# Optimization experiments

Measured on AMD Instinct MI355X. Metric: run time of the kernel, lower is better.

Reference implementation:

```python
import jax, jax.numpy as jnp
import numpy as np
from jax import lax

D, H, DH, F, K, L, N = 512, 8, 64, 2048, 31, 512, 16
EPS = 1e-5

def layer_norm(x, g, b):
    m = x.mean(-1, keepdims=True)
    v = ((x - m) ** 2).mean(-1, keepdims=True)
    return (x - m) / jnp.sqrt(v + EPS) * g + b

def swish(x):
    return x * jax.nn.sigmoid(x)

def ffn(x, w1, b1, w2, b2):
    return swish(x @ w1.T + b1) @ w2.T + b2

def rel_shift(x):
    # x: (N,H,T,2T-1) -> (N,H,T,T); out[...,i,j] = x[...,i, T-1-i+j]
    T = x.shape[2]
    rows = jnp.arange(T)[:, None]
    cols = (T - 1) - rows + jnp.arange(T)[None, :]
    return x[:, :, rows, cols]

def rel_attn(x, pos_emb, in_w, in_b, out_w, out_b, pos_w, bu, bv):
    Lq, Nb, E = x.shape
    qkv = x @ in_w.T + in_b  # (L,N,3E)
    q, k, v = jnp.split(qkv, 3, axis=-1)
    q = q.reshape(Lq, Nb, H, DH).transpose(1, 2, 0, 3)  # (N,H,L,DH)
    k = k.reshape(Lq, Nb, H, DH).transpose(1, 2, 0, 3)
    v = v.reshape(Lq, Nb, H, DH).transpose(1, 2, 0, 3)
    p = (pos_emb[0] @ pos_w.T).reshape(-1, H, DH).transpose(1, 0, 2)  # (H,2L-1,DH)
    scaling = DH ** -0.5
    q_u = q + bu[None, :, None, :]
    q_v = q + bv[None, :, None, :]
    matrix_ac = jnp.einsum('nhld,nhsd->nhls', q_u, k)        # (N,H,L,L)
    matrix_bd = jnp.einsum('nhld,hmd->nhlm', q_v, p)         # (N,H,L,2L-1)
    matrix_bd = rel_shift(matrix_bd)                         # (N,H,L,L)
    attn = jax.nn.softmax((matrix_ac + matrix_bd) * scaling, axis=-1)
    out = jnp.einsum('nhls,nhsd->nhld', attn, v)
    out = out.transpose(2, 0, 1, 3).reshape(Lq, Nb, E)
    return out @ out_w.T + out_b

def conv_module(x, pw1_w, pw1_b, dw_w, dw_b, g, b, mean, var, pw2_w, pw2_b):
    # x: (L,N,C) -> (N,C,L)
    y = x.transpose(1, 2, 0)
    y = jnp.einsum('ncl,oc->nol', y, pw1_w) + pw1_b[None, :, None]
    a, gate = jnp.split(y, 2, axis=1)
    y = a * jax.nn.sigmoid(gate)  # GLU over channel dim
    pad = (K - 1) // 2
    y = lax.conv_general_dilated(y, dw_w[:, None, :], (1,), [(pad, pad)],
                                 feature_group_count=D,
                                 dimension_numbers=('NCH', 'OIH', 'NCH'))
    y = y + dw_b[None, :, None]
    # BatchNorm1d in eval mode with running stats
    y = (y - mean[None, :, None]) / jnp.sqrt(var[None, :, None] + EPS)
    y = y * g[None, :, None] + b[None, :, None]
    y = swish(y)
    y = jnp.einsum('ncl,oc->nol', y, pw2_w) + pw2_b[None, :, None]
    return y.transpose(2, 0, 1)  # back to (L,N,C)

def setup_inputs() -> dict:
    key = jax.random.key(0)
    ks = iter(jax.random.split(key, 64))
    def nrm(shape, s=0.02):
        return jax.random.normal(next(ks), shape, dtype=jnp.float32) * s
    return {
        'src': jax.random.normal(next(ks), (L, N, D), dtype=jnp.float32),
        'pos_emb': jax.random.normal(next(ks), (1, 2 * L - 1, D), dtype=jnp.float32),
        'ffm_w1': nrm((F, D)), 'ffm_b1': jnp.zeros((F,), jnp.float32),
        'ffm_w2': nrm((D, F)), 'ffm_b2': jnp.zeros((D,), jnp.float32),
        'ff_w1': nrm((F, D)), 'ff_b1': jnp.zeros((F,), jnp.float32),
        'ff_w2': nrm((D, F)), 'ff_b2': jnp.zeros((D,), jnp.float32),
        'in_proj_w': nrm((3 * D, D)), 'in_proj_b': jnp.zeros((3 * D,), jnp.float32),
        'out_proj_w': nrm((D, D)), 'out_proj_b': jnp.zeros((D,), jnp.float32),
        'pos_w': nrm((D, D)),
        'pos_bias_u': nrm((H, DH)), 'pos_bias_v': nrm((H, DH)),
        'conv_pw1_w': nrm((2 * D, D)), 'conv_pw1_b': jnp.zeros((2 * D,), jnp.float32),
        'conv_dw_w': nrm((D, K)), 'conv_dw_b': jnp.zeros((D,), jnp.float32),
        'bn_gamma': jnp.ones((D,), jnp.float32), 'bn_beta': jnp.zeros((D,), jnp.float32),
        'bn_mean': jnp.zeros((D,), jnp.float32), 'bn_var': jnp.ones((D,), jnp.float32),
        'conv_pw2_w': nrm((D, D)), 'conv_pw2_b': jnp.zeros((D,), jnp.float32),
        'ln_ffm_g': jnp.ones((D,), jnp.float32), 'ln_ffm_b': jnp.zeros((D,), jnp.float32),
        'ln_mha_g': jnp.ones((D,), jnp.float32), 'ln_mha_b': jnp.zeros((D,), jnp.float32),
        'ln_conv_g': jnp.ones((D,), jnp.float32), 'ln_conv_b': jnp.zeros((D,), jnp.float32),
        'ln_ff_g': jnp.ones((D,), jnp.float32), 'ln_ff_b': jnp.zeros((D,), jnp.float32),
        'ln_final_g': jnp.ones((D,), jnp.float32), 'ln_final_b': jnp.zeros((D,), jnp.float32),
    }

def reference(src, pos_emb, ffm_w1, ffm_b1, ffm_w2, ffm_b2, ff_w1, ff_b1, ff_w2, ff_b2,
              in_proj_w, in_proj_b, out_proj_w, out_proj_b, pos_w, pos_bias_u, pos_bias_v,
              conv_pw1_w, conv_pw1_b, conv_dw_w, conv_dw_b, bn_gamma, bn_beta, bn_mean, bn_var,
              conv_pw2_w, conv_pw2_b, ln_ffm_g, ln_ffm_b, ln_mha_g, ln_mha_b, ln_conv_g, ln_conv_b,
              ln_ff_g, ln_ff_b, ln_final_g, ln_final_b):
    # pre-norm conformer block, ff_scale = 0.5, dropout omitted (eval)
    x = src
    x = x + 0.5 * ffn(layer_norm(x, ln_ffm_g, ln_ffm_b), ffm_w1, ffm_b1, ffm_w2, ffm_b2)
    x = x + rel_attn(layer_norm(x, ln_mha_g, ln_mha_b), pos_emb,
                     in_proj_w, in_proj_b, out_proj_w, out_proj_b,
                     pos_w, pos_bias_u, pos_bias_v)
    x = x + conv_module(layer_norm(x, ln_conv_g, ln_conv_b),
                        conv_pw1_w, conv_pw1_b, conv_dw_w, conv_dw_b,
                        bn_gamma, bn_beta, bn_mean, bn_var, conv_pw2_w, conv_pw2_b)
    x = x + 0.5 * ffn(layer_norm(x, ln_ff_g, ln_ff_b), ff_w1, ff_b1, ff_w2, ff_b2)
    return layer_norm(x, ln_final_g, ln_final_b)
```

## Files before the change

### kernel.cpp

```cpp
#include <hip/hip_runtime.h>
#include <cstdint>
#include <cstddef>

typedef unsigned short u16;
typedef __attribute__((ext_vector_type(4))) float f32x4;
typedef __attribute__((ext_vector_type(8))) short bf16x8;
typedef __attribute__((ext_vector_type(8))) unsigned short u16x8;

__device__ __forceinline__ float sigm(float x) { return 1.f / (1.f + __expf(-x)); }
__device__ __forceinline__ float bf2f(u16 u) {
    union { unsigned int i; float f; } c; c.i = ((unsigned int)u) << 16; return c.f;
}
__device__ __forceinline__ u16 f2bf(float f) {
    union { float f; unsigned int i; } c; c.f = f;
    unsigned int x = c.i;
    x += 0x7fffu + ((x >> 16) & 1u);
    return (u16)(x >> 16);
}


__global__ void castall_k(const float* __restrict__ s0, const float* __restrict__ s1,
                          const float* __restrict__ s2, const float* __restrict__ s3,
                          const float* __restrict__ s4, const float* __restrict__ s5,
                          const float* __restrict__ s6, const float* __restrict__ s7,
                          const float* __restrict__ s8, const float* __restrict__ s9,
                          u16* __restrict__ dst) {
    int i = blockIdx.x * 256 + threadIdx.x;
    if (i >= 6815232) return;
    const float* s; int off;
    if      (i < 1048576) { s = s0; off = 0; }
    else if (i < 2097152) { s = s1; off = 1048576; }
    else if (i < 3145728) { s = s2; off = 2097152; }
    else if (i < 4194304) { s = s3; off = 3145728; }
    else if (i < 4980736) { s = s4; off = 4194304; }
    else if (i < 5242880) { s = s5; off = 4980736; }
    else if (i < 5767168) { s = s6; off = 5242880; }
    else if (i < 6029312) { s = s7; off = 5767168; }
    else if (i < 6291456) { s = s8; off = 6029312; }
    else                  { s = s9; off = 6291456; }
    dst[i] = f2bf(s[i - off]);
}

template <bool OUTBF>
__global__ __launch_bounds__(256) void ln512_k(const float* __restrict__ x,
                                               const float* __restrict__ g,
                                               const float* __restrict__ b,
                                               void* __restrict__ outv) {
    int row = blockIdx.x * 4 + (threadIdx.x >> 6);
    int lane = threadIdx.x & 63;
    const float* xr = x + (size_t)row * 512 + lane * 8;
    float4 v0 = *(const float4*)(xr);
    float4 v1 = *(const float4*)(xr + 4);
    float va[8] = {v0.x, v0.y, v0.z, v0.w, v1.x, v1.y, v1.z, v1.w};
    float s = 0.f;
#pragma unroll
    for (int t = 0; t < 8; t++) s += va[t];
#pragma unroll
    for (int o = 32; o > 0; o >>= 1) s += __shfl_xor(s, o);
    float m = s * (1.0f / 512.0f);
    float q = 0.f;
#pragma unroll
    for (int t = 0; t < 8; t++) { float d = va[t] - m; q += d * d; }
#pragma unroll
    for (int o = 32; o > 0; o >>= 1) q += __shfl_xor(q, o);
    float inv = rsqrtf(q * (1.0f / 512.0f) + 1e-5f);
    int cb = lane * 8;
    if (OUTBF) {
        u16* o = (u16*)outv + (size_t)row * 512 + cb;
#pragma unroll
        for (int t = 0; t < 8; t++)
            o[t] = f2bf((va[t] - m) * inv * g[cb + t] + b[cb + t]);
    } else {
        float* o = (float*)outv + (size_t)row * 512 + cb;
#pragma unroll
        for (int t = 0; t < 8; t++)
            o[t] = (va[t] - m) * inv * g[cb + t] + b[cb + t];
    }
}

__global__ __launch_bounds__(512) void mgemm_k(
    const u16* __restrict__ A, const u16* __restrict__ B, const float* __restrict__ bias,
    const float* __restrict__ add, void* __restrict__ Cv,
    int M, int Nn, int Kk, float coef, int act, int outbf) {
    __shared__ u16 lA[2][4096];
    __shared__ u16 lB[2][4096];
    int tid = threadIdx.x;
    int half = tid >> 8;
    int t128 = tid & 255;
    int lane = tid & 63;
    int w = (tid >> 6) & 3;
    int wm = (w >> 1) * 64, wn = (w & 1) * 64;
    int m0 = blockIdx.x << 7, n0 = blockIdx.y << 7;
    int Kh = Kk >> 1;
    int kbase = half * Kh;

    f32x4 acc[4][4];
#pragma unroll
    for (int i = 0; i < 4; i++)
#pragma unroll
        for (int j = 0; j < 4; j++) acc[i][j] = (f32x4){0.f, 0.f, 0.f, 0.f};

    int srow = t128 >> 2;
    int scol = (t128 & 3) << 3;
    const u16* gA = A + (size_t)(m0 + srow) * Kk + kbase + scol;
    const u16* gB = B + (size_t)(n0 + srow) * Kk + kbase + scol;
    int lso = t128 * 8;

    int lra = wm * 32 + (lane & 15) * 32 + (lane >> 4) * 8;
    int lrb = wn * 32 + (lane & 15) * 32 + (lane >> 4) * 8;

    for (int k0 = 0; k0 < Kh; k0 += 32) {
        __builtin_amdgcn_global_load_lds(
            (const __attribute__((address_space(1))) void*)(gA + k0),
            (__attribute__((address_space(3))) void*)(lA[half] + lso), 16, 0, 0);
        __builtin_amdgcn_global_load_lds(
            (const __attribute__((address_space(1))) void*)(gA + (size_t)64 * Kk + k0),
            (__attribute__((address_space(3))) void*)(lA[half] + 2048 + lso), 16, 0, 0);
        __builtin_amdgcn_global_load_lds(
            (const __attribute__((address_space(1))) void*)(gB + k0),
            (__attribute__((address_space(3))) void*)(lB[half] + lso), 16, 0, 0);
        __builtin_amdgcn_global_load_lds(
            (const __attribute__((address_space(1))) void*)(gB + (size_t)64 * Kk + k0),
            (__attribute__((address_space(3))) void*)(lB[half] + 2048 + lso), 16, 0, 0);
        __syncthreads();
        bf16x8 af[4], bf[4];
#pragma unroll
        for (int t = 0; t < 4; t++) {
            af[t] = *(const bf16x8*)(lA[half] + lra + t * 512);
            bf[t] = *(const bf16x8*)(lB[half] + lrb + t * 512);
        }
#pragma unroll
        for (int i = 0; i < 4; i++)
#pragma unroll
            for (int j = 0; j < 4; j++)
                acc[i][j] = __builtin_amdgcn_mfma_f32_16x16x32_bf16(af[i], bf[j], acc[i][j], 0, 0, 0);
        __syncthreads();
    }

    float* red = (float*)lA;
#pragma unroll
    for (int rr = 0; rr < 4; rr++) {
        if (half == 1) {
#pragma unroll
            for (int j = 0; j < 4; j++)
                *(f32x4*)(red + ((w * 64 + lane) * 16 + j * 4)) = acc[rr][j];
        }
        __syncthreads();
        if (half == 0) {
#pragma unroll
            for (int j = 0; j < 4; j++) {
                f32x4 o = *(const f32x4*)(red + ((w * 64 + lane) * 16 + j * 4));
                acc[rr][j] += o;
            }
        }
        __syncthreads();
    }

    if (half == 0) {
        int rbase = (lane >> 4) * 4;
        int ncol = lane & 15;
#pragma unroll
        for (int i = 0; i < 4; i++) {
#pragma unroll
            for (int j = 0; j < 4; j++) {
                int n = n0 + wn + j * 16 + ncol;
                float bv = bias ? bias[n] : 0.f;
#pragma unroll
                for (int r = 0; r < 4; r++) {
                    int m = m0 + wm + i * 16 + rbase + r;
                    float c = acc[i][j][r] + bv;
                    if (act == 1) c *= sigm(c);
                    size_t o = (size_t)m * Nn + n;
                    if (add) c = add[o] + coef * c;
                    if (outbf) ((u16*)Cv)[o] = f2bf(c);
                    else ((float*)Cv)[o] = c;
                }
            }
        }
    }
}

__global__ __launch_bounds__(256) void posb_k(const u16* __restrict__ A,
                                              const u16* __restrict__ B,
                                              u16* __restrict__ Pbf) {
    __shared__ u16 lA[4096];
    __shared__ u16 lB[4096];
    const int Kk = 512;
    int tid = threadIdx.x;
    int lane = tid & 63, w = tid >> 6;
    int wm = (w >> 1) * 64, wn = (w & 1) * 64;
    int m0 = blockIdx.x << 7, n0 = blockIdx.y << 7;

    f32x4 acc[4][4];
#pragma unroll
    for (int i = 0; i < 4; i++)
#pragma unroll
        for (int j = 0; j < 4; j++) acc[i][j] = (f32x4){0.f, 0.f, 0.f, 0.f};

    int srow = tid >> 2;
    int scol = (tid & 3) << 3;
    int ar0 = m0 + srow;       if (ar0 > 1022) ar0 = 1022;
    int ar1 = m0 + 64 + srow;  if (ar1 > 1022) ar1 = 1022;
    const u16* gA0 = A + (size_t)ar0 * Kk + scol;
    const u16* gA1 = A + (size_t)ar1 * Kk + scol;
    const u16* gB = B + (size_t)(n0 + srow) * Kk + scol;
    int lso = tid * 8;
    int lra = wm * 32 + (lane & 15) * 32 + (lane >> 4) * 8;
    int lrb = wn * 32 + (lane & 15) * 32 + (lane >> 4) * 8;

    for (int k0 = 0; k0 < Kk; k0 += 32) {
        __builtin_amdgcn_global_load_lds(
            (const __attribute__((address_space(1))) void*)(gA0 + k0),
            (__attribute__((address_space(3))) void*)(lA + lso), 16, 0, 0);
        __builtin_amdgcn_global_load_lds(
            (const __attribute__((address_space(1))) void*)(gA1 + k0),
            (__attribute__((address_space(3))) void*)(lA + 2048 + lso), 16, 0, 0);
        __builtin_amdgcn_global_load_lds(
            (const __attribute__((address_space(1))) void*)(gB + k0),
            (__attribute__((address_space(3))) void*)(lB + lso), 16, 0, 0);
        __builtin_amdgcn_global_load_lds(
            (const __attribute__((address_space(1))) void*)(gB + (size_t)64 * Kk + k0),
            (__attribute__((address_space(3))) void*)(lB + 2048 + lso), 16, 0, 0);
        __syncthreads();
        bf16x8 af[4], bf[4];
#pragma unroll
        for (int t = 0; t < 4; t++) {
            af[t] = *(const bf16x8*)(lA + lra + t * 512);
            bf[t] = *(const bf16x8*)(lB + lrb + t * 512);
        }
#pragma unroll
        for (int i = 0; i < 4; i++)
#pragma unroll
            for (int j = 0; j < 4; j++)
                acc[i][j] = __builtin_amdgcn_mfma_f32_16x16x32_bf16(af[i], bf[j], acc[i][j], 0, 0, 0);
        __syncthreads();
    }

    int rbase = (lane >> 4) * 4;
    int ncol = lane & 15;
#pragma unroll
    for (int i = 0; i < 4; i++) {
#pragma unroll
        for (int j = 0; j < 4; j++) {
            int n = n0 + wn + j * 16 + ncol;
            int h = n >> 6, d = n & 63;
#pragma unroll
            for (int r = 0; r < 4; r++) {
                int m = m0 + wm + i * 16 + rbase + r;
                u16 val = (m < 1023) ? f2bf(acc[i][j][r]) : (u16)0;
                Pbf[(((size_t)(h * 1024 + m)) << 6) + d] = val;
            }
        }
    }
}

__global__ __launch_bounds__(256) void fattn_k(
    const u16* __restrict__ QU, const u16* __restrict__ QV,
    const u16* __restrict__ Kb, const u16* __restrict__ Pbf,
    const u16* __restrict__ VT, u16* __restrict__ ctx) {
    __shared__ u16 arr[26496];
    u16* sB = arr;
    u16* sV = arr;
    u16* sRect = arr + 16896;
    u16* sP = arr + 16896;
    u16* sQ = arr + 25344;
    u16* sCtx = arr + 25344;
    float* sRed = (float*)(arr + 26368);

    int tid = threadIdx.x;
    int lane = tid & 63, w = tid >> 6;
    int quad = lane >> 4, col = lane & 15;
    int nh = blockIdx.x, h = nh & 7, nb = nh >> 3;
    int m0 = blockIdx.y << 4;
    int nlo = 496 - m0;

    if (tid < 128)
        __builtin_amdgcn_global_load_lds(
            (const __attribute__((address_space(1))) void*)(QV + (((size_t)nh * 512 + m0 + (tid >> 3)) << 6) + ((tid & 7) << 3)),
            (__attribute__((address_space(3))) void*)(sQ + tid * 8), 16, 0, 0);
    f32x4 bdacc[9];
#pragma unroll
    for (int i = 0; i < 9; i++) bdacc[i] = (f32x4){0.f, 0.f, 0.f, 0.f};
    const u16* Pb = Pbf + ((size_t)h << 16);
    for (int ks = 0; ks < 2; ks++) {
#pragma unroll
        for (int s = 0; s < 8; s++) {
            int row = (s << 6) + (tid >> 2);
            __builtin_amdgcn_global_load_lds(
                (const __attribute__((address_space(1))) void*)(Pb + (((size_t)(nlo + row)) << 6) + (ks << 5) + ((tid & 3) << 3)),
                (__attribute__((address_space(3))) void*)(sB + (s << 11) + tid * 8), 16, 0, 0);
        }
        if (tid < 64) {
            int row = 512 + (tid >> 2);
            __builtin_amdgcn_global_load_lds(
                (const __attribute__((address_space(1))) void*)(Pb + (((size_t)(nlo + row)) << 6) + (ks << 5) + ((tid & 3) << 3)),
                (__attribute__((address_space(3))) void*)(sB + (8 << 11) + tid * 8), 16, 0, 0);
        }
        __syncthreads();
        bf16x8 a = *(const bf16x8*)(sQ + col * 64 + (ks << 5) + quad * 8);
#pragma unroll
        for (int idx = 0; idx < 9; idx++) {
            int nt = w + (idx << 2);
            if (nt < 33) {
                bf16x8 b = *(const bf16x8*)(sB + ((nt * 16 + col) << 5) + quad * 8);
                bdacc[idx] = __builtin_amdgcn_mfma_f32_16x16x32_bf16(a, b, bdacc[idx], 0, 0, 0);
            }
        }
        __syncthreads();
    }
#pragma unroll
    for (int idx = 0; idx < 9; idx++) {
        int nt = w + (idx << 2);
        if (nt < 33) {
            int c = nt * 16 + col;
#pragma unroll
            for (int r = 0; r < 4; r++) {
                int ml = quad * 4 + r;
                int j = c + ml - 15;
                if (j >= 0 && j < 512)
                    sRect[ml * 524 + j] = f2bf(bdacc[idx][r]);
            }
        }
    }
    __syncthreads();

    if (tid < 128)
        __builtin_amdgcn_global_load_lds(
            (const __attribute__((address_space(1))) void*)(QU + (((size_t)nh * 512 + m0 + (tid >> 3)) << 6) + ((tid & 7) << 3)),
            (__attribute__((address_space(3))) void*)(sQ + tid * 8), 16, 0, 0);
    f32x4 ac[8];
#pragma unroll
    for (int i = 0; i < 8; i++) ac[i] = (f32x4){0.f, 0.f, 0.f, 0.f};
    const u16* Kz = Kb + ((size_t)nh << 15);
    for (int ks = 0; ks < 2; ks++) {
#pragma unroll
        for (int s = 0; s < 8; s++) {
            int row = (s << 6) + (tid >> 2);
            __builtin_amdgcn_global_load_lds(
                (const __attribute__((address_space(1))) void*)(Kz + ((size_t)row << 6) + (ks << 5) + ((tid & 3) << 3)),
                (__attribute__((address_space(3))) void*)(sB + (s << 11) + tid * 8), 16, 0, 0);
        }
        __syncthreads();
        bf16x8 a = *(const bf16x8*)(sQ + col * 64 + (ks << 5) + quad * 8);
#pragma unroll
        for (int jt = 0; jt < 8; jt++) {
            bf16x8 b = *(const bf16x8*)(sB + (((w << 7) + jt * 16 + col) << 5) + quad * 8);
            ac[jt] = __builtin_amdgcn_mfma_f32_16x16x32_bf16(a, b, ac[jt], 0, 0, 0);
        }
        __syncthreads();
    }

    float rmax[4];
#pragma unroll
    for (int r = 0; r < 4; r++) rmax[r] = -1e30f;
#pragma unroll
    for (int jt = 0; jt < 8; jt++) {
        int j = (w << 7) + jt * 16 + col;
#pragma unroll
        for (int r = 0; r < 4; r++) {
            int ml = quad * 4 + r;
            float v = (ac[jt][r] + bf2f(sRect[ml * 524 + j])) * 0.125f;
            ac[jt][r] = v;
            rmax[r] = fmaxf(rmax[r], v);
        }
    }
#pragma unroll
    for (int o = 1; o <= 8; o <<= 1)
#pragma unroll
        for (int r = 0; r < 4; r++) rmax[r] = fmaxf(rmax[r], __shfl_xor(rmax[r], o));
    if (col == 0)
#pragma unroll
        for (int r = 0; r < 4; r++) sRed[(quad * 4 + r) * 4 + w] = rmax[r];
    __syncthreads();
    float gmax[4], psum[4];
#pragma unroll
    for (int r = 0; r < 4; r++) {
        int ml = quad * 4 + r;
        gmax[r] = fmaxf(fmaxf(sRed[ml * 4 + 0], sRed[ml * 4 + 1]),
                        fmaxf(sRed[ml * 4 + 2], sRed[ml * 4 + 3]));
        psum[r] = 0.f;
    }
    __syncthreads();
#pragma unroll
    for (int jt = 0; jt < 8; jt++)
#pragma unroll
        for (int r = 0; r < 4; r++) {
            float e = __expf(ac[jt][r] - gmax[r]);
            ac[jt][r] = e;
            psum[r] += e;
        }
#pragma unroll
    for (int o = 1; o <= 8; o <<= 1)
#pragma unroll
        for (int r = 0; r < 4; r++) psum[r] += __shfl_xor(psum[r], o);
    if (col == 0)
#pragma unroll
        for (int r = 0; r < 4; r++) sRed[(quad * 4 + r) * 4 + w] = psum[r];
    __syncthreads();
    float rinv[4];
#pragma unroll
    for (int r = 0; r < 4; r++) {
        int ml = quad * 4 + r;
        rinv[r] = 1.f / (sRed[ml * 4 + 0] + sRed[ml * 4 + 1] + sRed[ml * 4 + 2] + sRed[ml * 4 + 3]);
    }

#pragma unroll
    for (int jt = 0; jt < 8; jt++) {
        int j = (w << 7) + jt * 16 + col;
#pragma unroll
        for (int r = 0; r < 4; r++)
            sP[(quad * 4 + r) * 520 + j] = f2bf(ac[jt][r] * rinv[r]);
    }

    const u16* Vz = VT + ((size_t)nh << 15);
    f32x4 cacc = (f32x4){0.f, 0.f, 0.f, 0.f};
    for (int kc = 0; kc < 2; kc++) {
#pragma unroll
        for (int s = 0; s < 8; s++) {
            int d = (s << 3) + (tid >> 5);
            int chunk = (tid & 31) ^ (d & 7);
            __builtin_amdgcn_global_load_lds(
                (const __attribute__((address_space(1))) void*)(Vz + ((size_t)d << 9) + (kc << 8) + (chunk << 3)),
                (__attribute__((address_space(3))) void*)(sV + (s << 11) + tid * 8), 16, 0, 0);
        }
        __syncthreads();
#pragma unroll
        for (int s2 = 0; s2 < 8; s2++) {
            bf16x8 a = *(const bf16x8*)(sP + col * 520 + (kc << 8) + (s2 << 5) + quad * 8);
            int row = (w << 4) + col;
            int ch = ((s2 << 2) + quad) ^ (col & 7);
            bf16x8 b = *(const bf16x8*)(sV + (row << 8) + (ch << 3));
            cacc = __builtin_amdgcn_mfma_f32_16x16x32_bf16(a, b, cacc, 0, 0, 0);
        }
        __syncthreads();
    }

#pragma unroll
    for (int r = 0; r < 4; r++)
        sCtx[(quad * 4 + r) * 64 + (w << 4) + col] = f2bf(cacc[r]);
    __syncthreads();
    if (tid < 128) {
        int row = tid >> 3, seg = tid & 7;
        u16* dst = ctx + (((size_t)((m0 + row) * 16 + nb)) << 9) + (h << 6) + seg * 8;
        *(uint4*)dst = *(const uint4*)(sCtx + row * 64 + seg * 8);
    }
}

__global__ __launch_bounds__(256) void repack_k(const u16* __restrict__ qkv,
                                                const float* __restrict__ bu,
                                                const float* __restrict__ bv,
                                                u16* __restrict__ QU, u16* __restrict__ QV,
                                                u16* __restrict__ Kb, u16* __restrict__ VT) {
    __shared__ u16 sV[64 * 72];
    int nh = blockIdx.x, h = nh & 7, n = nh >> 3;
    int l0 = blockIdx.y << 6;
    int tid = threadIdx.x;
    int d8 = (tid & 7) << 3;
    float bub[8], bvb[8];
#pragma unroll
    for (int e = 0; e < 8; e++) {
        bub[e] = bu[h * 64 + d8 + e];
        bvb[e] = bv[h * 64 + d8 + e];
    }
#pragma unroll
    for (int rep = 0; rep < 2; rep++) {
        int ll = (tid >> 3) + rep * 32;
        int l = l0 + ll;
        size_t base = (size_t)(l * 16 + n) * 1536 + h * 64 + d8;
        u16x8 q = *(const u16x8*)(qkv + base);
        u16x8 k = *(const u16x8*)(qkv + base + 512);
        u16x8 v = *(const u16x8*)(qkv + base + 1024);
        u16x8 qu, qv;
#pragma unroll
        for (int e = 0; e < 8; e++) {
            float qf = bf2f(q[e]);
            qu[e] = f2bf(qf + bub[e]);
            qv[e] = f2bf(qf + bvb[e]);
        }
        size_t o = ((size_t)nh * 512 + l) * 64 + d8;
        *(u16x8*)(QU + o) = qu;
        *(u16x8*)(QV + o) = qv;
        *(u16x8*)(Kb + o) = k;
        *(u16x8*)(sV + ll * 72 + d8) = v;
    }
    __syncthreads();
    int d = tid >> 2, ls = (tid & 3) << 4;
    u16 tmp[16];
#pragma unroll
    for (int e = 0; e < 16; e++) tmp[e] = sV[(ls + e) * 72 + d];
    u16* dst = VT + ((size_t)nh * 64 + d) * 512 + l0 + ls;
    *(u16x8*)(dst) = *(const u16x8*)(tmp);
    *(u16x8*)(dst + 8) = *(const u16x8*)(tmp + 8);
}

__global__ void glu_k(const u16* __restrict__ pw1o, u16* __restrict__ g) {
    int e = blockIdx.x * 256 + threadIdx.x;
    int t = e >> 9, c = e & 511;
    float a = bf2f(pw1o[(size_t)t * 1024 + c]);
    float ga = bf2f(pw1o[(size_t)t * 1024 + 512 + c]);
    g[e] = f2bf(a * sigm(ga));
}

__global__ __launch_bounds__(256) void dwconv_k(
    const u16* __restrict__ g, const float* __restrict__ w, const float* __restrict__ wb,
    const float* __restrict__ bng, const float* __restrict__ bnb, const float* __restrict__ bnm,
    const float* __restrict__ bnv, u16* __restrict__ out) {
    int idx = blockIdx.x * 256 + threadIdx.x;
    int c = idx & 511;
    int t = idx >> 9;
    int n = t & 15, l0 = (t >> 4) << 4;
    float win[46];
#pragma unroll
    for (int q = 0; q < 46; q++) {
        int ll = l0 - 15 + q;
        win[q] = (ll >= 0 && ll < 512) ? bf2f(g[((size_t)(ll * 16 + n) << 9) + c]) : 0.f;
    }
    float wgt[31];
#pragma unroll
    for (int k = 0; k < 31; k++) wgt[k] = w[c * 31 + k];
    float ivg = rsqrtf(bnv[c] + 1e-5f) * bng[c];
    float mc = bnm[c], bc = bnb[c], wbc = wb[c];
#pragma unroll
    for (int r = 0; r < 16; r++) {
        float acc = 0.f;
#pragma unroll
        for (int k = 0; k < 31; k++) acc += wgt[k] * win[r + k];
        acc += wbc;
        float y = (acc - mc) * ivg + bc;
        y = y * sigm(y);
        out[((size_t)((l0 + r) * 16 + n) << 9) + c] = f2bf(y);
    }
}

extern "C" void kernel_launch(void* const* d_in, const int* in_sizes, int n_in,
                              void* d_out, int out_size, void* d_ws, size_t ws_size,
                              hipStream_t stream) {
    const float* src      = (const float*)d_in[0];
    const float* pos_emb  = (const float*)d_in[1];
    const float* ffm_w1   = (const float*)d_in[2];
    const float* ffm_b1   = (const float*)d_in[3];
    const float* ffm_w2   = (const float*)d_in[4];
    const float* ffm_b2   = (const float*)d_in[5];
    const float* ff_w1    = (const float*)d_in[6];
    const float* ff_b1    = (const float*)d_in[7];
    const float* ff_w2    = (const float*)d_in[8];
    const float* ff_b2    = (const float*)d_in[9];
    const float* in_w     = (const float*)d_in[10];
    const float* in_b     = (const float*)d_in[11];
    const float* out_w    = (const float*)d_in[12];
    const float* out_b    = (const float*)d_in[13];
    const float* pos_w    = (const float*)d_in[14];
    const float* bu       = (const float*)d_in[15];
    const float* bv       = (const float*)d_in[16];
    const float* pw1_w    = (const float*)d_in[17];
    const float* pw1_b    = (const float*)d_in[18];
    const float* dw_w     = (const float*)d_in[19];
    const float* dw_b     = (const float*)d_in[20];
    const float* bng      = (const float*)d_in[21];
    const float* bnb      = (const float*)d_in[22];
    const float* bnm      = (const float*)d_in[23];
    const float* bnv      = (const float*)d_in[24];
    const float* pw2_w    = (const float*)d_in[25];
    const float* pw2_b    = (const float*)d_in[26];
    const float* ln_ffm_g = (const float*)d_in[27];
    const float* ln_ffm_b = (const float*)d_in[28];
    const float* ln_mha_g = (const float*)d_in[29];
    const float* ln_mha_b = (const float*)d_in[30];
    const float* ln_cv_g  = (const float*)d_in[31];
    const float* ln_cv_b  = (const float*)d_in[32];
    const float* ln_ff_g  = (const float*)d_in[33];
    const float* ln_ff_b  = (const float*)d_in[34];
    const float* ln_fin_g = (const float*)d_in[35];
    const float* ln_fin_b = (const float*)d_in[36];
    (void)in_sizes; (void)n_in; (void)out_size; (void)ws_size;

    const size_t MEG = 1048576;
    u16* U = (u16*)d_ws;
    float* xA = (float*)U;
    u16* Pbf = U;
    float* xB = (float*)(U + 8 * MEG);
    u16* LNB = U + 16 * MEG;
    u16* BIG = U + 20 * MEG;
    u16* QU = U + 36 * MEG;
    u16* QV = U + 40 * MEG;
    u16* Kb = U + 44 * MEG;
    u16* VT = U + 48 * MEG;
    u16* WB = U + 52 * MEG;
    u16* w_ffm1 = WB;
    u16* w_ffm2 = WB + 1 * MEG;
    u16* w_ff1  = WB + 2 * MEG;
    u16* w_ff2  = WB + 3 * MEG;
    u16* w_in   = WB + 4 * MEG;
    u16* w_out  = WB + 4 * MEG + 786432;
    u16* w_pw1  = WB + 5 * MEG;
    u16* w_pw2  = WB + 5 * MEG + 524288;
    u16* w_pos  = WB + 6029312;
    u16* w_pe   = WB + 6291456;
    u16* CTX = LNB;
    u16* GLU = QU;
    u16* CACT = QV;

    castall_k<<<26622, 256, 0, stream>>>(ffm_w1, ffm_w2, ff_w1, ff_w2, in_w, out_w,
                                         pw1_w, pw2_w, pos_w, pos_emb, WB);

    ln512_k<true><<<2048, 256, 0, stream>>>(src, ln_ffm_g, ln_ffm_b, LNB);
    mgemm_k<<<dim3(64, 16), 512, 0, stream>>>(LNB, w_ffm1, ffm_b1, nullptr, BIG,
                                              8192, 2048, 512, 0.f, 1, 1);
    mgemm_k<<<dim3(64, 4), 512, 0, stream>>>(BIG, w_ffm2, ffm_b2, src, xB,
                                             8192, 512, 2048, 0.5f, 0, 0);

    ln512_k<true><<<2048, 256, 0, stream>>>(xB, ln_mha_g, ln_mha_b, LNB);
    posb_k<<<dim3(8, 4), 256, 0, stream>>>(w_pe, w_pos, Pbf);
    mgemm_k<<<dim3(64, 12), 512, 0, stream>>>(LNB, w_in, in_b, nullptr, BIG,
                                              8192, 1536, 512, 0.f, 0, 1);
    repack_k<<<dim3(128, 8), 256, 0, stream>>>(BIG, bu, bv, QU, QV, Kb, VT);
    fattn_k<<<dim3(128, 32), 256, 0, stream>>>(QU, QV, Kb, Pbf, VT, CTX);
    mgemm_k<<<dim3(64, 4), 512, 0, stream>>>(CTX, w_out, out_b, xB, xA,
                                             8192, 512, 512, 1.f, 0, 0);

    ln512_k<true><<<2048, 256, 0, stream>>>(xA, ln_cv_g, ln_cv_b, LNB);
    mgemm_k<<<dim3(64, 8), 512, 0, stream>>>(LNB, w_pw1, pw1_b, nullptr, BIG,
                                             8192, 1024, 512, 0.f, 0, 1);
    glu_k<<<16384, 256, 0, stream>>>(BIG, GLU);
    dwconv_k<<<1024, 256, 0, stream>>>(GLU, dw_w, dw_b, bng, bnb, bnm, bnv, CACT);
    mgemm_k<<<dim3(64, 4), 512, 0, stream>>>(CACT, w_pw2, pw2_b, xA, xB,
                                             8192, 512, 512, 1.f, 0, 0);

    ln512_k<true><<<2048, 256, 0, stream>>>(xB, ln_ff_g, ln_ff_b, LNB);
    mgemm_k<<<dim3(64, 16), 512, 0, stream>>>(LNB, w_ff1, ff_b1, nullptr, BIG,
                                              8192, 2048, 512, 0.f, 1, 1);
    mgemm_k<<<dim3(64, 4), 512, 0, stream>>>(BIG, w_ff2, ff_b2, xB, xA,
                                             8192, 512, 2048, 0.5f, 0, 0);

    ln512_k<false><<<2048, 256, 0, stream>>>(xA, ln_fin_g, ln_fin_b, (float*)d_out);
}
```

Baseline: 617.3 us.

## Double attention query tile to 32 rows and load K/V/P fragments directly from global

The fused relative-position attention kernel now handles 32 query rows per block instead of 16, halving the grid. The K, V and positional B-operands are read straight from global memory into registers instead of being staged through LDS with global_load_lds and barriers. Each B fragment now feeds two MFMAs, one per 16-row query half, doubling reuse of the key, value and position loads. This removes most LDS staging traffic and barriers and shrinks shared memory, but raises register pressure and relies on uncoalesced per-lane global loads hitting cache, with fewer blocks available to hide latency.

```diff
diff --git a/kernel.cpp b/kernel.cpp
--- a/kernel.cpp
+++ b/kernel.cpp
@@ -258,188 +258,188 @@
     const u16* __restrict__ QU, const u16* __restrict__ QV,
     const u16* __restrict__ Kb, const u16* __restrict__ Pbf,
     const u16* __restrict__ VT, u16* __restrict__ ctx) {
-    __shared__ u16 arr[26496];
-    u16* sB = arr;
-    u16* sV = arr;
-    u16* sRect = arr + 16896;
-    u16* sP = arr + 16896;
-    u16* sQ = arr + 25344;
-    u16* sCtx = arr + 25344;
-    float* sRed = (float*)(arr + 26368);
+    __shared__ u16 arr[19072];
+    u16* sRect = arr;
+    u16* sP = arr;
+    u16* sCtx = arr + 16768;
+    float* sRed = (float*)(arr + 18816);
 
     int tid = threadIdx.x;
     int lane = tid & 63, w = tid >> 6;
     int quad = lane >> 4, col = lane & 15;
     int nh = blockIdx.x, h = nh & 7, nb = nh >> 3;
-    int m0 = blockIdx.y << 4;
-    int nlo = 496 - m0;
-
-    if (tid < 128)
-        __builtin_amdgcn_global_load_lds(
-            (const __attribute__((address_space(1))) void*)(QV + (((size_t)nh * 512 + m0 + (tid >> 3)) << 6) + ((tid & 7) << 3)),
-            (__attribute__((address_space(3))) void*)(sQ + tid * 8), 16, 0, 0);
-    f32x4 bdacc[9];
-#pragma unroll
-    for (int i = 0; i < 9; i++) bdacc[i] = (f32x4){0.f, 0.f, 0.f, 0.f};
-    const u16* Pb = Pbf + ((size_t)h << 16);
-    for (int ks = 0; ks < 2; ks++) {
-#pragma unroll
-        for (int s = 0; s < 8; s++) {
-            int row = (s << 6) + (tid >> 2);
-            __builtin_amdgcn_global_load_lds(
-                (const __attribute__((address_space(1))) void*)(Pb + (((size_t)(nlo + row)) << 6) + (ks << 5) + ((tid & 3) << 3)),
-                (__attribute__((address_space(3))) void*)(sB + (s << 11) + tid * 8), 16, 0, 0);
-        }
-        if (tid < 64) {
-            int row = 512 + (tid >> 2);
-            __builtin_amdgcn_global_load_lds(
-                (const __attribute__((address_space(1))) void*)(Pb + (((size_t)(nlo + row)) << 6) + (ks << 5) + ((tid & 3) << 3)),
-                (__attribute__((address_space(3))) void*)(sB + (8 << 11) + tid * 8), 16, 0, 0);
-        }
-        __syncthreads();
-        bf16x8 a = *(const bf16x8*)(sQ + col * 64 + (ks << 5) + quad * 8);
-#pragma unroll
-        for (int idx = 0; idx < 9; idx++) {
-            int nt = w + (idx << 2);
-            if (nt < 33) {
-                bf16x8 b = *(const bf16x8*)(sB + ((nt * 16 + col) << 5) + quad * 8);
-                bdacc[idx] = __builtin_amdgcn_mfma_f32_16x16x32_bf16(a, b, bdacc[idx], 0, 0, 0);
-            }
-        }
-        __syncthreads();
-    }
+    int m0 = blockIdx.y << 5;
+    int nlo = 480 - m0;
+
+    const u16* QVz = QV + ((size_t)nh << 15);
+    const u16* QUz = QU + ((size_t)nh << 15);
+    const u16* Kz  = Kb + ((size_t)nh << 15);
+    const u16* Vz  = VT + ((size_t)nh << 15);
+    const u16* Pb  = Pbf + ((size_t)h << 16);
+
+    bf16x8 av[2][2];
+#pragma unroll
+    for (int ks = 0; ks < 2; ks++)
+#pragma unroll
+        for (int t = 0; t < 2; t++)
+            av[ks][t] = *(const bf16x8*)(QVz + ((size_t)(m0 + t * 16 + col) << 6) + (ks << 5) + quad * 8);
 #pragma unroll
     for (int idx = 0; idx < 9; idx++) {
         int nt = w + (idx << 2);
-        if (nt < 33) {
-            int c = nt * 16 + col;
+        if (nt < 34) {
+            int crow = nt * 16 + col;
+            const u16* pb = Pb + ((size_t)(nlo + crow) << 6) + quad * 8;
+            f32x4 b0 = (f32x4){0.f, 0.f, 0.f, 0.f};
+            f32x4 b1 = (f32x4){0.f, 0.f, 0.f, 0.f};
+#pragma unroll
+            for (int ks = 0; ks < 2; ks++) {
+                bf16x8 bfr = *(const bf16x8*)(pb + (ks << 5));
+                b0 = __builtin_amdgcn_mfma_f32_16x16x32_bf16(av[ks][0], bfr, b0, 0, 0, 0);
+                b1 = __builtin_amdgcn_mfma_f32_16x16x32_bf16(av[ks][1], bfr, b1, 0, 0, 0);
+            }
 #pragma unroll
             for (int r = 0; r < 4; r++) {
-                int ml = quad * 4 + r;
-                int j = c + ml - 15;
-                if (j >= 0 && j < 512)
-                    sRect[ml * 524 + j] = f2bf(bdacc[idx][r]);
-            }
+                int ml0 = quad * 4 + r;
+                int j0 = crow + ml0 - 31;
+                if (j0 >= 0 && j0 < 512) sRect[ml0 * 524 + j0] = f2bf(b0[r]);
+                int ml1 = ml0 + 16;
+                int j1 = crow + ml1 - 31;
+                if (j1 >= 0 && j1 < 512) sRect[ml1 * 524 + j1] = f2bf(b1[r]);
+            }
+        }
+    }
+
+    bf16x8 au[2][2];
+#pragma unroll
+    for (int ks = 0; ks < 2; ks++)
+#pragma unroll
+        for (int t = 0; t < 2; t++)
+            au[ks][t] = *(const bf16x8*)(QUz + ((size_t)(m0 + t * 16 + col) << 6) + (ks << 5) + quad * 8);
+    f32x4 ac[2][8];
+#pragma unroll
+    for (int t = 0; t < 2; t++)
+#pragma unroll
+        for (int jt = 0; jt < 8; jt++) ac[t][jt] = (f32x4){0.f, 0.f, 0.f, 0.f};
+#pragma unroll
+    for (int jt = 0; jt < 8; jt++) {
+        const u16* kp = Kz + ((size_t)((w << 7) + jt * 16 + col) << 6) + quad * 8;
+#pragma unroll
+        for (int ks = 0; ks < 2; ks++) {
+            bf16x8 bfr = *(const bf16x8*)(kp + (ks << 5));
+            ac[0][jt] = __builtin_amdgcn_mfma_f32_16x16x32_bf16(au[ks][0], bfr, ac[0][jt], 0, 0, 0);
+            ac[1][jt] = __builtin_amdgcn_mfma_f32_16x16x32_bf16(au[ks][1], bfr, ac[1][jt], 0, 0, 0);
         }
     }
     __syncthreads();
 
-    if (tid < 128)
-        __builtin_amdgcn_global_load_lds(
-            (const __attribute__((address_space(1))) void*)(QU + (((size_t)nh * 512 + m0 + (tid >> 3)) << 6) + ((tid & 7) << 3)),
-            (__attribute__((address_space(3))) void*)(sQ + tid * 8), 16, 0, 0);
-    f32x4 ac[8];
-#pragma unroll
-    for (int i = 0; i < 8; i++) ac[i] = (f32x4){0.f, 0.f, 0.f, 0.f};
-    const u16* Kz = Kb + ((size_t)nh << 15);
-    for (int ks = 0; ks < 2; ks++) {
-#pragma unroll
-        for (int s = 0; s < 8; s++) {
-            int row = (s << 6) + (tid >> 2);
-            __builtin_amdgcn_global_load_lds(
-                (const __attribute__((address_space(1))) void*)(Kz + ((size_t)row << 6) + (ks << 5) + ((tid & 3) << 3)),
-                (__attribute__((address_space(3))) void*)(sB + (s << 11) + tid * 8), 16, 0, 0);
-        }
-        __syncthreads();
-        bf16x8 a = *(const bf16x8*)(sQ + col * 64 + (ks << 5) + quad * 8);
-#pragma unroll
-        for (int jt = 0; jt < 8; jt++) {
-            bf16x8 b = *(const bf16x8*)(sB + (((w << 7) + jt * 16 + col) << 5) + quad * 8);
-            ac[jt] = __builtin_amdgcn_mfma_f32_16x16x32_bf16(a, b, ac[jt], 0, 0, 0);
-        }
-        __syncthreads();
-    }
-
-    float rmax[4];
-#pragma unroll
-    for (int r = 0; r < 4; r++) rmax[r] = -1e30f;
+    float rmax[2][4];
+#pragma unroll
+    for (int t = 0; t < 2; t++)
+#pragma unroll
+        for (int r = 0; r < 4; r++) rmax[t][r] = -1e30f;
 #pragma unroll
     for (int jt = 0; jt < 8; jt++) {
         int j = (w << 7) + jt * 16 + col;
 #pragma unroll
+        for (int t = 0; t < 2; t++)
+#pragma unroll
+            for (int r = 0; r < 4; r++) {
+                int ml = t * 16 + quad * 4 + r;
+                float v = (ac[t][jt][r] + bf2f(sRect[ml * 524 + j])) * 0.125f;
+                ac[t][jt][r] = v;
+                rmax[t][r] = fmaxf(rmax[t][r], v);
+            }
+    }
+#pragma unroll
+    for (int o = 1; o <= 8; o <<= 1)
+#pragma unroll
+        for (int t = 0; t < 2; t++)
+#pragma unroll
+            for (int r = 0; r < 4; r++) rmax[t][r] = fmaxf(rmax[t][r], __shfl_xor(rmax[t][r], o));
+    if (col == 0)
+#pragma unroll
+        for (int t = 0; t < 2; t++)
+#pragma unroll
+            for (int r = 0; r < 4; r++) sRed[(t * 16 + quad * 4 + r) * 4 + w] = rmax[t][r];
+    __syncthreads();
+    float gmax[2][4], psum[2][4];
+#pragma unroll
+    for (int t = 0; t < 2; t++)
+#pragma unroll
         for (int r = 0; r < 4; r++) {
-            int ml = quad * 4 + r;
-            float v = (ac[jt][r] + bf2f(sRect[ml * 524 + j])) * 0.125f;
-            ac[jt][r] = v;
-            rmax[r] = fmaxf(rmax[r], v);
-        }
-    }
+            int ml = t * 16 + quad * 4 + r;
+            gmax[t][r] = fmaxf(fmaxf(sRed[ml * 4 + 0], sRed[ml * 4 + 1]),
+                               fmaxf(sRed[ml * 4 + 2], sRed[ml * 4 + 3]));
+            psum[t][r] = 0.f;
+        }
+    __syncthreads();
+#pragma unroll
+    for (int jt = 0; jt < 8; jt++)
+#pragma unroll
+        for (int t = 0; t < 2; t++)
+#pragma unroll
+            for (int r = 0; r < 4; r++) {
+                float e = __expf(ac[t][jt][r] - gmax[t][r]);
+                ac[t][jt][r] = e;
+                psum[t][r] += e;
+            }
 #pragma unroll
     for (int o = 1; o <= 8; o <<= 1)
 #pragma unroll
-        for (int r = 0; r < 4; r++) rmax[r] = fmaxf(rmax[r], __shfl_xor(rmax[r], o));
+        for (int t = 0; t < 2; t++)
+#pragma unroll
+            for (int r = 0; r < 4; r++) psum[t][r] += __shfl_xor(psum[t][r], o);
     if (col == 0)
 #pragma unroll
-        for (int r = 0; r < 4; r++) sRed[(quad * 4 + r) * 4 + w] = rmax[r];
+        for (int t = 0; t < 2; t++)
+#pragma unroll
+            for (int r = 0; r < 4; r++) sRed[(t * 16 + quad * 4 + r) * 4 + w] = psum[t][r];
     __syncthreads();
-    float gmax[4], psum[4];
-#pragma unroll
-    for (int r = 0; r < 4; r++) {
-        int ml = quad * 4 + r;
-        gmax[r] = fmaxf(fmaxf(sRed[ml * 4 + 0], sRed[ml * 4 + 1]),
-                        fmaxf(sRed[ml * 4 + 2], sRed[ml * 4 + 3]));
-        psum[r] = 0.f;
-    }
-    __syncthreads();
-#pragma unroll
-    for (int jt = 0; jt < 8; jt++)
+    float rinv[2][4];
+#pragma unroll
+    for (int t = 0; t < 2; t++)
 #pragma unroll
         for (int r = 0; r < 4; r++) {
-            float e = __expf(ac[jt][r] - gmax[r]);
-            ac[jt][r] = e;
-            psum[r] += e;
-        }
-#pragma unroll
-    for (int o = 1; o <= 8; o <<= 1)
-#pragma unroll
-        for (int r = 0; r < 4; r++) psum[r] += __shfl_xor(psum[r], o);
-    if (col == 0)
-#pragma unroll
-        for (int r = 0; r < 4; r++) sRed[(quad * 4 + r) * 4 + w] = psum[r];
-    __syncthreads();
-    float rinv[4];
-#pragma unroll
-    for (int r = 0; r < 4; r++) {
-        int ml = quad * 4 + r;
-        rinv[r] = 1.f / (sRed[ml * 4 + 0] + sRed[ml * 4 + 1] + sRed[ml * 4 + 2] + sRed[ml * 4 + 3]);
-    }
+            int ml = t * 16 + quad * 4 + r;
+            rinv[t][r] = 1.f / (sRed[ml * 4 + 0] + sRed[ml * 4 + 1] + sRed[ml * 4 + 2] + sRed[ml * 4 + 3]);
+        }
 
 #pragma unroll
     for (int jt = 0; jt < 8; jt++) {
         int j = (w << 7) + jt * 16 + col;
 #pragma unroll
+        for (int t = 0; t < 2; t++)
+#pragma unroll
+            for (int r = 0; r < 4; r++)
+                sP[(t * 16 + quad * 4 + r) * 520 + j] = f2bf(ac[t][jt][r] * rinv[t][r]);
+    }
+    __syncthreads();
+
+    f32x4 cacc[2];
+    cacc[0] = (f32x4){0.f, 0.f, 0.f, 0.f};
+    cacc[1] = (f32x4){0.f, 0.f, 0.f, 0.f};
+    {
+        const u16* vp = Vz + ((size_t)((w << 4) + col) << 9) + quad * 8;
+#pragma unroll
+        for (int kc = 0; kc < 2; kc++)
+#pragma unroll
+            for (int s2 = 0; s2 < 8; s2++) {
+                int ko = (kc << 8) + (s2 << 5);
+                bf16x8 a0 = *(const bf16x8*)(sP + col * 520 + ko + quad * 8);
+                bf16x8 a1 = *(const bf16x8*)(sP + (col + 16) * 520 + ko + quad * 8);
+                bf16x8 bfr = *(const bf16x8*)(vp + ko);
+                cacc[0] = __builtin_amdgcn_mfma_f32_16x16x32_bf16(a0, bfr, cacc[0], 0, 0, 0);
+                cacc[1] = __builtin_amdgcn_mfma_f32_16x16x32_bf16(a1, bfr, cacc[1], 0, 0, 0);
+            }
+    }
+
+#pragma unroll
+    for (int t = 0; t < 2; t++)
+#pragma unroll
         for (int r = 0; r < 4; r++)
-            sP[(quad * 4 + r) * 520 + j] = f2bf(ac[jt][r] * rinv[r]);
-    }
-
-    const u16* Vz = VT + ((size_t)nh << 15);
-    f32x4 cacc = (f32x4){0.f, 0.f, 0.f, 0.f};
-    for (int kc = 0; kc < 2; kc++) {
-#pragma unroll
-        for (int s = 0; s < 8; s++) {
-            int d = (s << 3) + (tid >> 5);
-            int chunk = (tid & 31) ^ (d & 7);
-            __builtin_amdgcn_global_load_lds(
-                (const __attribute__((address_space(1))) void*)(Vz + ((size_t)d << 9) + (kc << 8) + (chunk << 3)),
-                (__attribute__((address_space(3))) void*)(sV + (s << 11) + tid * 8), 16, 0, 0);
-        }
-        __syncthreads();
-#pragma unroll
-        for (int s2 = 0; s2 < 8; s2++) {
-            bf16x8 a = *(const bf16x8*)(sP + col * 520 + (kc << 8) + (s2 << 5) + quad * 8);
-            int row = (w << 4) + col;
-            int ch = ((s2 << 2) + quad) ^ (col & 7);
-            bf16x8 b = *(const bf16x8*)(sV + (row << 8) + (ch << 3));
-            cacc = __builtin_amdgcn_mfma_f32_16x16x32_bf16(a, b, cacc, 0, 0, 0);
-        }
-        __syncthreads();
-    }
-
-#pragma unroll
-    for (int r = 0; r < 4; r++)
-        sCtx[(quad * 4 + r) * 64 + (w << 4) + col] = f2bf(cacc[r]);
+            sCtx[(t * 16 + quad * 4 + r) * 64 + (w << 4) + col] = f2bf(cacc[t][r]);
     __syncthreads();
-    if (tid < 128) {
+    {
         int row = tid >> 3, seg = tid & 7;
         u16* dst = ctx + (((size_t)((m0 + row) * 16 + nb)) << 9) + (h << 6) + seg * 8;
         *(uint4*)dst = *(const uint4*)(sCtx + row * 64 + seg * 8);
@@ -614,7 +614,7 @@
     mgemm_k<<<dim3(64, 12), 512, 0, stream>>>(LNB, w_in, in_b, nullptr, BIG,
                                               8192, 1536, 512, 0.f, 0, 1);
     repack_k<<<dim3(128, 8), 256, 0, stream>>>(BIG, bu, bv, QU, QV, Kb, VT);
-    fattn_k<<<dim3(128, 32), 256, 0, stream>>>(QU, QV, Kb, Pbf, VT, CTX);
+    fattn_k<<<dim3(128, 16), 256, 0, stream>>>(QU, QV, Kb, Pbf, VT, CTX);
     mgemm_k<<<dim3(64, 4), 512, 0, stream>>>(CTX, w_out, out_b, xB, xA,
                                              8192, 512, 512, 1.f, 0, 0);
 
```

Result: no change. 620.1 us (+0.4%).
